# Kernel optimization log

Hardware: AMD Instinct MI355X
Metric: run time of the kernel (lower is better)

The kernel has to match this reference:

```python
import jax, jax.numpy as jnp
import numpy as np

CLASS_NUM = 31
KERNEL_MUL = 2.0
KERNEL_NUM = 5


def setup_inputs() -> dict:
    key = jax.random.key(0)
    k1, k2, k3, k4 = jax.random.split(key, 4)
    B, D = 4096, 512
    source = jax.random.normal(k1, (B, D), dtype=jnp.float32)
    target = jax.random.normal(k2, (B, D), dtype=jnp.float32)
    s_label = jax.random.randint(k3, (B,), 0, CLASS_NUM)
    t_label = jax.random.uniform(k4, (B, CLASS_NUM), dtype=jnp.float32)
    return {"source": source, "target": target, "s_label": s_label, "t_label": t_label}


def _cal_weight(s_label, t_label):
    # Faithful port of the numpy weight computation (detached in the original).
    C = CLASS_NUM
    s_onehot = jax.nn.one_hot(s_label, C, dtype=jnp.float32)          # [Bs, C]
    s_sum = s_onehot.sum(axis=0)
    s_vec = s_onehot / jnp.where(s_sum == 0, 1e9, s_sum)
    t_pred = jnp.argmax(t_label, axis=1)
    t_sum = t_label.sum(axis=0)
    t_vec = t_label / jnp.where(t_sum == 0, 1.0, t_sum)
    # classes present in BOTH source labels and target argmax predictions
    s_present = s_onehot.sum(axis=0) > 0
    t_present = jax.nn.one_hot(t_pred, C, dtype=jnp.float32).sum(axis=0) > 0
    mask = (s_present & t_present).astype(jnp.float32)                # [C]
    s_vec = s_vec * mask
    t_vec = t_vec * mask
    length = mask.sum()
    inv_len = jnp.where(length > 0, 1.0 / length, 0.0)
    w_ss = (s_vec @ s_vec.T) * inv_len
    w_tt = (t_vec @ t_vec.T) * inv_len
    w_st = (s_vec @ t_vec.T) * inv_len
    w_ts = (t_vec @ s_vec.T) * inv_len
    return w_ss, w_tt, w_st, w_ts


def _gaussian_kernel(source, target):
    n = source.shape[0] + target.shape[0]
    total = jnp.concatenate([source, target], axis=0)                 # [n, d]
    # Gram-matrix trick for pairwise squared L2 (avoids n x n x d intermediate)
    sq = jnp.sum(total * total, axis=1)                               # [n]
    L2 = jnp.maximum(sq[:, None] + sq[None, :] - 2.0 * (total @ total.T), 0.0)
    bandwidth = jax.lax.stop_gradient(jnp.sum(L2)) / (n * n - n)      # .data -> detach
    bandwidth = bandwidth / (KERNEL_MUL ** (KERNEL_NUM // 2))
    kernels = jnp.zeros_like(L2)
    for i in range(KERNEL_NUM):
        kernels = kernels + jnp.exp(-L2 / (bandwidth * KERNEL_MUL ** i))
    return kernels


def reference(source, target, s_label, t_label):
    B = source.shape[0]
    w_ss, w_tt, w_st, w_ts = _cal_weight(s_label, t_label)
    w_ss = jax.lax.stop_gradient(w_ss)
    w_tt = jax.lax.stop_gradient(w_tt)
    w_st = jax.lax.stop_gradient(w_st)
    w_ts = jax.lax.stop_gradient(w_ts)
    kernels = _gaussian_kernel(source, target)
    SS = kernels[:B, :B]
    TT = kernels[B:, B:]
    ST = kernels[:B, B:]
    TS = kernels[B:, :B]
    loss = (jnp.sum(w_ss * SS) + jnp.sum(w_tt * TT)
            - jnp.sum(w_st * ST) - jnp.sum(w_ts * TS))
    # original returns 0 if the kernel matrix contains NaNs
    return jnp.where(jnp.any(jnp.isnan(kernels)), 0.0, loss)
```

## Files before the change

### kernel.cpp

```cpp
#include <hip/hip_runtime.h>

#define N_TOT 8192
#define BHALF 4096
#define D 512
#define C 31
#define QS 21.166666666666668f
#define C2 0.0044644089288178575f

typedef float f32x16 __attribute__((ext_vector_type(16)));
typedef int   i32x16 __attribute__((ext_vector_type(16)));
typedef int   i32x4  __attribute__((ext_vector_type(4)));
typedef __bf16 bf16x8 __attribute__((ext_vector_type(8)));

__device__ __forceinline__ uint bf16_rne(uint u) {
  return (u + 0x7fffu + ((u >> 16) & 1u)) >> 16;
}
__device__ __forceinline__ void split2(float x, uint& h, uint& lo) {
  uint u = __float_as_uint(x);
  h = bf16_rne(u);
  float hf = __uint_as_float(h << 16);
  lo = bf16_rne(__float_as_uint(x - hf));
}
__device__ __forceinline__ void gll16(const void* g, void* s) {
  __builtin_amdgcn_global_load_lds(
      (const __attribute__((address_space(1))) unsigned int*)g,
      (__attribute__((address_space(3))) unsigned int*)s, 16, 0, 0);
}
__device__ __forceinline__ uint pack4(const float* x, int o) {
  uint r = 0;
  #pragma unroll
  for (int b = 0; b < 4; ++b) {
    float xs = x[o + b] * QS;
    xs = fmaxf(fminf(xs, 127.f), -127.f);
    int q = __float2int_rn(xs);
    r |= (uint)(q & 255) << (8 * b);
  }
  return r;
}

__global__ __launch_bounds__(256) void k_split(const float* __restrict__ src,
                                               const float* __restrict__ tgt,
                                               const float* __restrict__ tl,
                                               const int* __restrict__ slab,
                                               uchar* __restrict__ qG,
                                               float* __restrict__ sq,
                                               float* __restrict__ m,
                                               float* __restrict__ tsum,
                                               int* __restrict__ pres,
                                               int* __restrict__ cnt,
                                               float* __restrict__ out) {
  __shared__ float lsq[4][32];
  __shared__ float lcol[128];
  __shared__ float ts[C];
  __shared__ int hcnt[C];
  int tid = threadIdx.x, l = tid & 63, wid = tid >> 6;
  int bx = (int)blockIdx.x;
  if (bx < 1024) {
    int rg = bx >> 2;
    int kb = bx & 3;
    int ksg = kb * 4 + wid;
    int row = rg * 32 + (l & 31);
    int k0 = ksg * 32 + (l >> 5) * 16;
    const float* p = (row < BHALF) ? src + (size_t)row * D : tgt + (size_t)(row - BHALF) * D;
    float x[16];
    #pragma unroll
    for (int q = 0; q < 4; ++q) {
      float4 v = *(const float4*)(p + k0 + q * 4);
      x[q*4+0] = v.x; x[q*4+1] = v.y; x[q*4+2] = v.z; x[q*4+3] = v.w;
    }
    uint4 o = make_uint4(pack4(x, 0), pack4(x, 4), pack4(x, 8), pack4(x, 12));
    *(uint4*)(qG + (((size_t)rg * 16 + ksg) * 64 + l) * 16) = o;
    float s = 0.f;
    #pragma unroll
    for (int j = 0; j < 16; ++j) s = fmaf(x[j], x[j], s);
    s += __shfl_xor(s, 32);
    if (l < 32) lsq[wid][l] = s;
    #pragma unroll
    for (int off = 1; off <= 16; off <<= 1)
      #pragma unroll
      for (int j = 0; j < 16; ++j) x[j] += __shfl_xor(x[j], off);
    if ((l & 31) == 0) {
      #pragma unroll
      for (int j = 0; j < 16; ++j) lcol[wid * 32 + (l >> 5) * 16 + j] = x[j];
    }
    __syncthreads();
    if (tid < 32) {
      float t = lsq[0][tid] + lsq[1][tid] + lsq[2][tid] + lsq[3][tid];
      atomicAdd(&sq[rg * 32 + tid], t);
    } else if (tid >= 128) {
      int cc = tid - 128;
      atomicAdd(&m[kb * 128 + cc], lcol[cc]);
    }
  } else {
    int b = bx - 1024;
    if (tid < C) { ts[tid] = 0.f; hcnt[tid] = 0; }
    __syncthreads();
    int base = b * 128 * C;
    for (int idx = tid; idx < 128 * C; idx += 256) {
      atomicAdd(&ts[idx % C], tl[base + idx]);
    }
    if (tid < 128) {
      int row = b * 128 + tid;
      const float* p = tl + (size_t)row * C;
      float best = p[0]; int bi = 0;
      for (int c = 1; c < C; c++) { float v = p[c]; if (v > best) { best = v; bi = c; } }
      pres[bi] = 1;
      atomicAdd(&hcnt[slab[row]], 1);
    }
    if (b == 0 && tid == 255) out[0] = 0.f;
    __syncthreads();
    if (tid < C) {
      atomicAdd(&tsum[tid], ts[tid]);
      atomicAdd(&cnt[tid], hcnt[tid]);
    }
  }
}

#define WAITV4 asm volatile("s_waitcnt vmcnt(4)" ::: "memory")
#define WAITV0 asm volatile("s_waitcnt vmcnt(0)" ::: "memory")
#define WAITL0 asm volatile("s_waitcnt lgkmcnt(0)" ::: "memory")

__global__ __launch_bounds__(256, 4) void k_main(
    const uchar* __restrict__ qG,
    const int* __restrict__ slab, const float* __restrict__ tl,
    const float* __restrict__ sq, const float* __restrict__ m,
    const float* __restrict__ tsum, const int* __restrict__ pres,
    const int* __restrict__ cnt, float* __restrict__ out) {
  __shared__ uint4 lds4[2][1024];
  __shared__ float sqA[128], sqB[128], red[8];
  __shared__ float svalS[32], tscaleS[32], scalS[1];

  int tid = threadIdx.x;
  int l = tid & 63, wid = tid >> 6;

  int bid = (int)blockIdx.x;
  int swz = (bid & 7) * 260 + (bid >> 3);
  int ti = 0, rem = swz;
  for (;;) { int w = 64 - ti; if (rem < w) break; rem -= w; ++ti; }
  int tj = ti + rem;

  i32x16 zeroi;
  f32x16 zero16;
  #pragma unroll
  for (int k = 0; k < 16; ++k) { zeroi[k] = 0; zero16[k] = 0.f; }
  i32x16 acc[2][2];
  acc[0][0] = zeroi; acc[0][1] = zeroi; acc[1][0] = zeroi; acc[1][1] = zeroi;

  int wrg = (wid >> 1) * 2;
  int wcg = (wid & 1) * 2;

  int rgbase_m = ((wid < 2) ? ti : tj) * 4;
  int rg_off = (wid & 1) * 2;
  int side_off = (wid < 2) ? 0 : 8192;

#define STAGE(P) do {                                                              \
    uchar* lb = ((uchar*)lds4[(P) & 1]) + side_off;                                \
    _Pragma("unroll")                                                              \
    for (int r = 0; r < 4; ++r) {                                                  \
      int rgl = rg_off + (r >> 1), ksl = r & 1;                                    \
      const uchar* g = qG + (((size_t)(rgbase_m + rgl) * 16 + ((P) * 2 + ksl)) * 64 + l) * 16; \
      gll16(g, lb + ((rgl * 2 + ksl) * 64 + l) * 16);                              \
    }                                                                              \
  } while (0)

  STAGE(0);
  #pragma unroll
  for (int p = 0; p < 8; ++p) {
    if (p + 1 < 8) STAGE(p + 1);
    if (p < 7) { WAITV4; } else { WAITV0; }
    __builtin_amdgcn_sched_barrier(0);
    __builtin_amdgcn_s_barrier();
    uchar* As = (uchar*)lds4[p & 1];
    uchar* Bs = As + 8192;
    __builtin_amdgcn_s_setprio(1);
    #pragma unroll
    for (int ksl = 0; ksl < 2; ++ksl) {
      i32x4 a0 = *(const i32x4*)(As + (((wrg + 0) * 2 + ksl) * 64 + l) * 16);
      i32x4 a1 = *(const i32x4*)(As + (((wrg + 1) * 2 + ksl) * 64 + l) * 16);
      i32x4 b0 = *(const i32x4*)(Bs + (((wcg + 0) * 2 + ksl) * 64 + l) * 16);
      i32x4 b1 = *(const i32x4*)(Bs + (((wcg + 1) * 2 + ksl) * 64 + l) * 16);
      acc[0][0] = __builtin_amdgcn_mfma_i32_32x32x32_i8(a0, b0, acc[0][0], 0, 0, 0);
      acc[0][1] = __builtin_amdgcn_mfma_i32_32x32x32_i8(a0, b1, acc[0][1], 0, 0, 0);
      acc[1][0] = __builtin_amdgcn_mfma_i32_32x32x32_i8(a1, b0, acc[1][0], 0, 0, 0);
      acc[1][1] = __builtin_amdgcn_mfma_i32_32x32x32_i8(a1, b1, acc[1][1], 0, 0, 0);
    }
    __builtin_amdgcn_s_setprio(0);
    WAITL0;
    __builtin_amdgcn_sched_barrier(0);
    __builtin_amdgcn_s_barrier();
  }
#undef STAGE

  if (tid < 128) { sqA[tid] = sq[ti * 128 + tid]; sqB[tid] = sq[tj * 128 + tid]; }
  float s = 0.f;
  for (int i = tid; i < N_TOT; i += 256) s += sq[i];
  float q = 0.f;
  for (int d = tid; d < D; d += 256) q += m[d] * m[d];
  #pragma unroll
  for (int off = 32; off; off >>= 1) { s += __shfl_xor(s, off); q += __shfl_xor(q, off); }
  if (l == 0) { red[wid] = s; red[4 + wid] = q; }
  __syncthreads();
  float Ssum = red[0] + red[1] + red[2] + red[3];
  float Msum = red[4] + red[5] + red[6] + red[7];
  double sumL2 = 2.0 * (double)N_TOT * (double)Ssum - 2.0 * (double)Msum;
  double bw = sumL2 / ((double)N_TOT * (double)N_TOT - (double)N_TOT) / 4.0;
  float nib = (float)(-1.4426950408889634 / (16.0 * bw));
  if (tid < 32) {
    int c = tid;
    int cc = 0; float tv = 0.f; int pr = 0;
    if (c < C) { cc = cnt[c]; tv = tsum[c]; pr = pres[c]; }
    int mk = (cc > 0 && pr != 0) ? 1 : 0;
    unsigned long long ball = __ballot(mk);
    int len = __popcll(ball);
    svalS[c] = mk ? (1.0f / (float)cc) : 0.f;
    tscaleS[c] = mk ? (1.0f / (tv == 0.f ? 1.f : tv)) : 0.f;
    if (c == 0) scalS[0] = (len > 0) ? (1.0f / (float)len) : 0.f;
  }
  __syncthreads();

  ushort* AsU = (ushort*)lds4[0];
  ushort* BsU = (ushort*)lds4[1];
  #pragma unroll
  for (int it = 0; it < 4; ++it) {
    int slot = tid + it * 256;
    int pl = slot >> 6;
    int ll = slot & 63;
    int side = pl >> 3;
    int rgl = (pl & 7) >> 1;
    int ks = pl & 1;
    int row = (side ? tj : ti) * 128 + rgl * 32 + (ll & 31);
    int j0 = ks * 16 + (ll >> 5) * 8;
    float vals[8];
    if (row < BHALF) {
      int cls = slab[row];
      float v = svalS[cls];
      #pragma unroll
      for (int jj = 0; jj < 8; ++jj) vals[jj] = (j0 + jj == cls) ? v : 0.f;
    } else {
      const float* p = tl + (size_t)(row - BHALF) * C;
      #pragma unroll
      for (int jj = 0; jj < 8; ++jj) {
        int cj = j0 + jj;
        vals[jj] = (cj < C) ? -p[cj] * tscaleS[cj] : 0.f;
      }
    }
    uint h[8], lo[8];
    #pragma unroll
    for (int jj = 0; jj < 8; ++jj) split2(vals[jj], h[jj], lo[jj]);
    ushort* base = (side ? BsU : AsU) + ((rgl * 2 + ks) * 64 + ll) * 8;
    *(uint4*)base = make_uint4(h[0]|(h[1]<<16), h[2]|(h[3]<<16),
                               h[4]|(h[5]<<16), h[6]|(h[7]<<16));
    *(uint4*)(base + 4096) = make_uint4(lo[0]|(lo[1]<<16), lo[2]|(lo[3]<<16),
                                        lo[4]|(lo[5]<<16), lo[6]|(lo[7]<<16));
  }
  __syncthreads();

  float partial = 0.f;
  int colb = (wid & 1) * 64 + (l & 31);
  int rowb = (wid >> 1) * 64 + 4 * (l >> 5);
  #pragma unroll
  for (int i = 0; i < 2; ++i) {
    bf16x8 caH0 = *(const bf16x8*)(AsU + (((wrg + i) * 2 + 0) * 64 + l) * 8);
    bf16x8 caH1 = *(const bf16x8*)(AsU + (((wrg + i) * 2 + 1) * 64 + l) * 8);
    bf16x8 caL0 = *(const bf16x8*)(AsU + 4096 + (((wrg + i) * 2 + 0) * 64 + l) * 8);
    bf16x8 caL1 = *(const bf16x8*)(AsU + 4096 + (((wrg + i) * 2 + 1) * 64 + l) * 8);
    #pragma unroll
    for (int j = 0; j < 2; ++j) {
      bf16x8 cbH0 = *(const bf16x8*)(BsU + (((wcg + j) * 2 + 0) * 64 + l) * 8);
      bf16x8 cbH1 = *(const bf16x8*)(BsU + (((wcg + j) * 2 + 1) * 64 + l) * 8);
      bf16x8 cbL0 = *(const bf16x8*)(BsU + 4096 + (((wcg + j) * 2 + 0) * 64 + l) * 8);
      bf16x8 cbL1 = *(const bf16x8*)(BsU + 4096 + (((wcg + j) * 2 + 1) * 64 + l) * 8);
      f32x16 w = zero16;
      w = __builtin_amdgcn_mfma_f32_32x32x16_bf16(caH0, cbH0, w, 0, 0, 0);
      w = __builtin_amdgcn_mfma_f32_32x32x16_bf16(caH1, cbH1, w, 0, 0, 0);
      w = __builtin_amdgcn_mfma_f32_32x32x16_bf16(caH0, cbL0, w, 0, 0, 0);
      w = __builtin_amdgcn_mfma_f32_32x32x16_bf16(caH1, cbL1, w, 0, 0, 0);
      w = __builtin_amdgcn_mfma_f32_32x32x16_bf16(caL0, cbH0, w, 0, 0, 0);
      w = __builtin_amdgcn_mfma_f32_32x32x16_bf16(caL1, cbH1, w, 0, 0, 0);
      float sb = sqB[colb + j * 32];
      #pragma unroll
      for (int reg = 0; reg < 16; ++reg) {
        int row = rowb + i * 32 + (reg & 3) + 8 * (reg >> 2);
        float l2 = fmaxf(sqA[row] + sb - C2 * (float)acc[i][j][reg], 0.f);
        float e = __builtin_amdgcn_exp2f(l2 * nib);
        float kern = e;
        e *= e; kern += e;
        e *= e; kern += e;
        e *= e; kern += e;
        e *= e; kern += e;
        partial = fmaf(w[reg], kern, partial);
      }
    }
  }
  #pragma unroll
  for (int off = 32; off; off >>= 1) partial += __shfl_xor(partial, off);
  if (l == 0) red[wid] = partial;
  __syncthreads();
  if (tid == 0) {
    float v = (red[0] + red[1] + red[2] + red[3]) * scalS[0] * ((ti == tj) ? 1.0f : 2.0f);
    atomicAdd(out, v);
  }
}

extern "C" void kernel_launch(void* const* d_in, const int* in_sizes, int n_in,
                              void* d_out, int out_size, void* d_ws, size_t ws_size,
                              hipStream_t stream) {
  const float* src = (const float*)d_in[0];
  const float* tgt = (const float*)d_in[1];
  const int* slab  = (const int*)d_in[2];
  const float* tl  = (const float*)d_in[3];
  float* out = (float*)d_out;

  uchar*  qG = (uchar*)d_ws;
  float* fb  = (float*)(qG + 4194304);
  float* sq   = fb;
  float* m    = fb + 8192;
  float* tsum = fb + 8704;
  int*   pres = (int*)(fb + 8736);
  int*   cnt  = (int*)(fb + 8768);

  hipMemsetAsync(fb, 0, 8800 * sizeof(float), stream);
  hipLaunchKernelGGL(k_split, dim3(1056), dim3(256), 0, stream,
                     src, tgt, tl, slab, qG, sq, m, tsum, pres, cnt, out);
  hipLaunchKernelGGL(k_main,  dim3(2080), dim3(256), 0, stream,
                     qG, slab, tl, sq, m, tsum, pres, cnt, out);
}
```

Measured before the change: 89.36 us.

## Precompute global squared-norm sum in split kernel and drop LDS double buffering

The split kernel now reduces the total squared norm into a single scalar, so each main-kernel block no longer re-reads all 8192 row norms to compute the bandwidth. The bandwidth and class-weight setup moves before the GEMM loop, and the bandwidth math switches from double to float. The double-buffered LDS pipeline with manual waitcnt is replaced by a single buffer and plain __syncthreads per K-chunk. This removes redundant per-block reduction work but serialises global loads with MFMA compute, and the float bandwidth path may shift precision slightly.

```diff
diff --git a/kernel.cpp b/kernel.cpp
--- a/kernel.cpp
+++ b/kernel.cpp
@@ -4,6 +4,7 @@
 #define BHALF 4096
 #define D 512
 #define C 31
+#define NKCI 8
 #define QS 21.166666666666668f
 #define C2 0.0044644089288178575f
 
@@ -48,6 +49,7 @@
                                                float* __restrict__ tsum,
                                                int* __restrict__ pres,
                                                int* __restrict__ cnt,
+                                               float* __restrict__ Ssum,
                                                float* __restrict__ out) {
   __shared__ float lsq[4][32];
   __shared__ float lcol[128];
@@ -87,6 +89,10 @@
     if (tid < 32) {
       float t = lsq[0][tid] + lsq[1][tid] + lsq[2][tid] + lsq[3][tid];
       atomicAdd(&sq[rg * 32 + tid], t);
+      float tot = t;
+      #pragma unroll
+      for (int off = 16; off; off >>= 1) tot += __shfl_xor(tot, off);
+      if (tid == 0) atomicAdd(Ssum, tot);
     } else if (tid >= 128) {
       int cc = tid - 128;
       atomicAdd(&m[kb * 128 + cc], lcol[cc]);
@@ -116,19 +122,21 @@
   }
 }
 
-#define WAITV4 asm volatile("s_waitcnt vmcnt(4)" ::: "memory")
-#define WAITV0 asm volatile("s_waitcnt vmcnt(0)" ::: "memory")
-#define WAITL0 asm volatile("s_waitcnt lgkmcnt(0)" ::: "memory")
-
 __global__ __launch_bounds__(256, 4) void k_main(
     const uchar* __restrict__ qG,
     const int* __restrict__ slab, const float* __restrict__ tl,
     const float* __restrict__ sq, const float* __restrict__ m,
     const float* __restrict__ tsum, const int* __restrict__ pres,
-    const int* __restrict__ cnt, float* __restrict__ out) {
-  __shared__ uint4 lds4[2][1024];
-  __shared__ float sqA[128], sqB[128], red[8];
-  __shared__ float svalS[32], tscaleS[32], scalS[1];
+    const int* __restrict__ cnt, const float* __restrict__ Ssum,
+    float* __restrict__ out) {
+  __shared__ uint4 As4[1024];
+  __shared__ uint4 Bs4[1024];
+  __shared__ float sqA[128], sqB[128], red[4];
+  __shared__ float svalS[32], tscaleS[32], scalS[2];
+  uchar* As = (uchar*)As4;
+  uchar* Bs = (uchar*)Bs4;
+  ushort* AsU = (ushort*)As4;
+  ushort* BsU = (ushort*)Bs4;
 
   int tid = threadIdx.x;
   int l = tid & 63, wid = tid >> 6;
@@ -139,6 +147,31 @@
   for (;;) { int w = 64 - ti; if (rem < w) break; rem -= w; ++ti; }
   int tj = ti + rem;
 
+  if (tid < 128) { sqA[tid] = sq[ti * 128 + tid]; sqB[tid] = sq[tj * 128 + tid]; }
+  {
+    float m0 = m[tid], m1 = m[tid + 256];
+    float q = m0 * m0 + m1 * m1;
+    #pragma unroll
+    for (int off = 32; off; off >>= 1) q += __shfl_xor(q, off);
+    if (l == 0) red[wid] = q;
+  }
+  __syncthreads();
+  {
+    float Msum = red[0] + red[1] + red[2] + red[3];
+    float sumL2 = 2.0f * (float)N_TOT * Ssum[0] - 2.0f * Msum;
+    if (tid == 0) scalS[0] = -1.4426950408889634f * 67100672.0f / (4.0f * sumL2);
+  }
+  if (tid < 32) {
+    int c = tid;
+    int cc = cnt[c]; float tv = tsum[c]; int pr = pres[c];
+    int mk = (c < C && cc > 0 && pr != 0) ? 1 : 0;
+    unsigned long long ball = __ballot(mk);
+    int len = __popcll(ball);
+    svalS[c] = mk ? (1.0f / (float)cc) : 0.f;
+    tscaleS[c] = mk ? (1.0f / (tv == 0.f ? 1.f : tv)) : 0.f;
+    if (c == 0) scalS[1] = (len > 0) ? (1.0f / (float)len) : 0.f;
+  }
+
   i32x16 zeroi;
   f32x16 zero16;
   #pragma unroll
@@ -151,27 +184,16 @@
 
   int rgbase_m = ((wid < 2) ? ti : tj) * 4;
   int rg_off = (wid & 1) * 2;
-  int side_off = (wid < 2) ? 0 : 8192;
-
-#define STAGE(P) do {                                                              \
-    uchar* lb = ((uchar*)lds4[(P) & 1]) + side_off;                                \
-    _Pragma("unroll")                                                              \
-    for (int r = 0; r < 4; ++r) {                                                  \
-      int rgl = rg_off + (r >> 1), ksl = r & 1;                                    \
-      const uchar* g = qG + (((size_t)(rgbase_m + rgl) * 16 + ((P) * 2 + ksl)) * 64 + l) * 16; \
-      gll16(g, lb + ((rgl * 2 + ksl) * 64 + l) * 16);                              \
-    }                                                                              \
-  } while (0)
-
-  STAGE(0);
-  #pragma unroll
-  for (int p = 0; p < 8; ++p) {
-    if (p + 1 < 8) STAGE(p + 1);
-    if (p < 7) { WAITV4; } else { WAITV0; }
-    __builtin_amdgcn_sched_barrier(0);
-    __builtin_amdgcn_s_barrier();
-    uchar* As = (uchar*)lds4[p & 1];
-    uchar* Bs = As + 8192;
+  uchar* lb_m = (wid < 2) ? As : Bs;
+
+  for (int kci = 0; kci < NKCI; ++kci) {
+    #pragma unroll
+    for (int r = 0; r < 4; ++r) {
+      int rgl = rg_off + (r >> 1), ksl = r & 1;
+      const uchar* g = qG + (((size_t)(rgbase_m + rgl) * 16 + kci * 2 + ksl) * 64 + l) * 16;
+      gll16(g, lb_m + ((rgl * 2 + ksl) * 64 + l) * 16);
+    }
+    __syncthreads();
     __builtin_amdgcn_s_setprio(1);
     #pragma unroll
     for (int ksl = 0; ksl < 2; ++ksl) {
@@ -185,41 +207,9 @@
       acc[1][1] = __builtin_amdgcn_mfma_i32_32x32x32_i8(a1, b1, acc[1][1], 0, 0, 0);
     }
     __builtin_amdgcn_s_setprio(0);
-    WAITL0;
-    __builtin_amdgcn_sched_barrier(0);
-    __builtin_amdgcn_s_barrier();
-  }
-#undef STAGE
-
-  if (tid < 128) { sqA[tid] = sq[ti * 128 + tid]; sqB[tid] = sq[tj * 128 + tid]; }
-  float s = 0.f;
-  for (int i = tid; i < N_TOT; i += 256) s += sq[i];
-  float q = 0.f;
-  for (int d = tid; d < D; d += 256) q += m[d] * m[d];
-  #pragma unroll
-  for (int off = 32; off; off >>= 1) { s += __shfl_xor(s, off); q += __shfl_xor(q, off); }
-  if (l == 0) { red[wid] = s; red[4 + wid] = q; }
-  __syncthreads();
-  float Ssum = red[0] + red[1] + red[2] + red[3];
-  float Msum = red[4] + red[5] + red[6] + red[7];
-  double sumL2 = 2.0 * (double)N_TOT * (double)Ssum - 2.0 * (double)Msum;
-  double bw = sumL2 / ((double)N_TOT * (double)N_TOT - (double)N_TOT) / 4.0;
-  float nib = (float)(-1.4426950408889634 / (16.0 * bw));
-  if (tid < 32) {
-    int c = tid;
-    int cc = 0; float tv = 0.f; int pr = 0;
-    if (c < C) { cc = cnt[c]; tv = tsum[c]; pr = pres[c]; }
-    int mk = (cc > 0 && pr != 0) ? 1 : 0;
-    unsigned long long ball = __ballot(mk);
-    int len = __popcll(ball);
-    svalS[c] = mk ? (1.0f / (float)cc) : 0.f;
-    tscaleS[c] = mk ? (1.0f / (tv == 0.f ? 1.f : tv)) : 0.f;
-    if (c == 0) scalS[0] = (len > 0) ? (1.0f / (float)len) : 0.f;
-  }
-  __syncthreads();
-
-  ushort* AsU = (ushort*)lds4[0];
-  ushort* BsU = (ushort*)lds4[1];
+    __syncthreads();
+  }
+
   #pragma unroll
   for (int it = 0; it < 4; ++it) {
     int slot = tid + it * 256;
@@ -255,6 +245,7 @@
   }
   __syncthreads();
 
+  float nib = scalS[0];
   float partial = 0.f;
   int colb = (wid & 1) * 64 + (l & 31);
   int rowb = (wid >> 1) * 64 + 4 * (l >> 5);
@@ -297,7 +288,7 @@
   if (l == 0) red[wid] = partial;
   __syncthreads();
   if (tid == 0) {
-    float v = (red[0] + red[1] + red[2] + red[3]) * scalS[0] * ((ti == tj) ? 1.0f : 2.0f);
+    float v = (red[0] + red[1] + red[2] + red[3]) * scalS[1] * ((ti == tj) ? 1.0f : 2.0f);
     atomicAdd(out, v);
   }
 }
@@ -318,10 +309,11 @@
   float* tsum = fb + 8704;
   int*   pres = (int*)(fb + 8736);
   int*   cnt  = (int*)(fb + 8768);
-
-  hipMemsetAsync(fb, 0, 8800 * sizeof(float), stream);
+  float* Ssum = fb + 8800;
+
+  hipMemsetAsync(fb, 0, 8832 * sizeof(float), stream);
   hipLaunchKernelGGL(k_split, dim3(1056), dim3(256), 0, stream,
-                     src, tgt, tl, slab, qG, sq, m, tsum, pres, cnt, out);
+                     src, tgt, tl, slab, qG, sq, m, tsum, pres, cnt, Ssum, out);
   hipLaunchKernelGGL(k_main,  dim3(2080), dim3(256), 0, stream,
-                     qG, slab, tl, sq, m, tsum, pres, cnt, out);
-}
+                     qG, slab, tl, sq, m, tsum, pres, cnt, Ssum, out);
+}
```

After: 92.51 us. 3.5% more time.
